# Kernel optimization log

Measured on AMD Instinct MI355X. Metric: run time of the kernel, lower is better.

## Reference

```python
import jax, jax.numpy as jnp
import numpy as np

B, T = 64, 64
HUMAN, IN = 64, 8
HS, ES, K = 1024, 1024, 7
PSI_H, PSI_LR = 1024, 30

_PAR_SHAPES = [(HS, HS), (HS,), (IN, HS), (HS, HUMAN), (IN, HUMAN - IN)]
_PAR_SIZES = [int(np.prod(s)) for s in _PAR_SHAPES]
N_PSI = int(sum(_PAR_SIZES))
_OFFS = np.cumsum([0] + _PAR_SIZES)


def setup_inputs() -> dict:
    key = jax.random.key(0)
    ks = jax.random.split(key, 16)
    def xav(k, shape):
        lim = float(np.sqrt(6.0 / (shape[0] + shape[1])))
        return jax.random.uniform(k, shape, minval=-lim, maxval=lim, dtype=jnp.float32)
    def uni(k, shape, s):
        return jax.random.uniform(k, shape, minval=-s, maxval=s, dtype=jnp.float32)
    se = float(1.0 / np.sqrt(ES))
    return {
        "inputs": jax.random.normal(ks[0], (B, T, IN), jnp.float32),
        "outputs": jax.random.normal(ks[1], (B, T, HUMAN), jnp.float32),
        "eps": jax.random.normal(ks[2], (B, K), jnp.float32),
        "enc_Wih": uni(ks[3], (3 * ES, HUMAN), se),
        "enc_Whh": uni(ks[4], (3 * ES, ES), se),
        "enc_bih": uni(ks[5], (3 * ES,), se),
        "enc_bhh": uni(ks[6], (3 * ES,), se),
        "to_mu": xav(ks[7], (ES, K)),
        "to_lsigma": xav(ks[8], (ES, K)),
        "to_lsigma_bias": -0.5 * jnp.ones((K,), jnp.float32),
        "W1": xav(ks[9], (K, PSI_H)),
        "b1": jnp.zeros((PSI_H,), jnp.float32),
        "W2": xav(ks[10], (PSI_H, PSI_LR)),
        "b2": jnp.zeros((PSI_LR,), jnp.float32),
        "W3": xav(ks[11], (PSI_LR, N_PSI)),
        "b3": jnp.zeros((N_PSI,), jnp.float32),
        "gru_Wih": xav(ks[12], (IN, 2 * HS)),
        "gru_Whh": xav(ks[13], (HS, 2 * HS)),
        "gru_bias": jnp.concatenate([jnp.zeros((HS,)), jnp.ones((HS,))]).astype(jnp.float32),
    }


def _gru_cell(h, x, Wih, Whh, bih, bhh):
    # torch.nn.GRUCell math, gate order (r, z, n)
    gx = x @ Wih.T + bih
    gh = h @ Whh.T + bhh
    xr, xz, xn = jnp.split(gx, 3, axis=-1)
    hr, hz, hn = jnp.split(gh, 3, axis=-1)
    r = jax.nn.sigmoid(xr + hr)
    z = jax.nn.sigmoid(xz + hz)
    n = jnp.tanh(xn + r * hn)
    return (1.0 - z) * n + z * h


def _split_psi(psi):
    # psi: [B, N_PSI] -> per-sample (Whh, bh, Wih, C, D)
    return [psi[:, _OFFS[i]:_OFFS[i + 1]].reshape((-1,) + _PAR_SHAPES[i]) for i in range(5)]


def reference(inputs, outputs, eps, enc_Wih, enc_Whh, enc_bih, enc_bhh,
              to_mu, to_lsigma, to_lsigma_bias, W1, b1, W2, b2, W3, b3,
              gru_Wih, gru_Whh, gru_bias):
    bsz = inputs.shape[0]
    # ---- encoder: GRUCell over time-major outputs ----
    out_tm = jnp.swapaxes(outputs, 0, 1)  # [T, B, HUMAN]
    h0 = jnp.zeros((bsz, ES), inputs.dtype)
    h_enc = _gru_cell(h0, out_tm[0], enc_Wih, enc_Whh, enc_bih, enc_bhh)
    def enc_step(h, x):
        h = _gru_cell(h, x, enc_Wih, enc_Whh, enc_bih, enc_bhh)
        return h, None
    h_enc, _ = jax.lax.scan(enc_step, h_enc, out_tm[1:])
    mu = h_enc @ to_mu                       # [B, K]
    logstd = h_enc @ to_lsigma + to_lsigma_bias
    z = mu + eps * jnp.exp(logstd)
    # ---- hypernetwork psi decoder ----
    psi = (jnp.tanh(z @ W1 + b1) @ W2 + b2) @ W3 + b3   # [B, N_PSI]
    Whh_b, bh_b, Wih_b, C_b, D_b = _split_psi(psi)
    # ---- per-sample GRU decoder, vectorized over batch, scan over time ----
    gx_all = jnp.einsum('bti,ij->tbj', inputs, gru_Wih)  # [T, B, 2*HS]
    xW_all = jnp.einsum('bti,bih->tbh', inputs, Wih_b)   # [T, B, HS]

    def dec_step(h, xs):
        gx_t, xW_t = xs
        pre = gx_t + h @ gru_Whh + gru_bias   # [B, 2*HS]
        z_t = jax.nn.sigmoid(pre[:, :HS])
        r_t = jax.nn.sigmoid(pre[:, HS:])
        hWhh = jnp.einsum('bh,bhk->bk', h, Whh_b) + bh_b
        eta = jnp.tanh(xW_t + r_t * jnp.tanh(hWhh))
        h_new = z_t * h + (1.0 - z_t) * eta
        return h_new, h_new

    state0 = jnp.zeros((bsz, HS), inputs.dtype)
    h_last, dec_seq = jax.lax.scan(dec_step, state0, (gx_all, xW_all))
    dec_seq = jnp.swapaxes(dec_seq, 0, 1)    # [B, T, HS]
    # ---- readout ----
    yhats = jnp.einsum('bth,bhm->btm', dec_seq, C_b)
    xD = jnp.einsum('bti,bim->btm', inputs, D_b)  # [B, T, HUMAN-IN]
    yhats = yhats + jnp.concatenate([jnp.zeros_like(inputs), xD], axis=-1)
    # residual output
    yhats = yhats + jnp.concatenate(
        [inputs, jnp.zeros((bsz, inputs.shape[1], HUMAN - IN), inputs.dtype)], axis=-1)
    states = jax.lax.stop_gradient(h_last)
    return yhats, mu, logstd, states
```

## Files before the change

kernel.cpp:

```cpp
#include <hip/hip_runtime.h>

namespace {
constexpr int nT = 64;
constexpr int nK = 7;
constexpr long N_PSI = 1123776;
constexpr long SZ_WHH = 1048576;
constexpr long REST_SZ = 75200;
constexpr long R_BH = 0;
constexpr long R_WIH = 1024;
constexpr long R_C = 9216;
constexpr long R_D = 74752;
constexpr int NCH = 32;
constexpr int CHR = 32;
constexpr long PHALF = (long)NCH * 64 * 1024;
}

typedef __attribute__((ext_vector_type(4))) unsigned short us4;
typedef __attribute__((ext_vector_type(2))) unsigned short us2;

__device__ __forceinline__ float b2f(unsigned short u) {
  return __uint_as_float(((unsigned int)u) << 16);
}
__device__ __forceinline__ unsigned short f2b(float f) {
  unsigned int u = __float_as_uint(f);
  return (unsigned short)((u + 0x7fffu + ((u >> 16) & 1u)) >> 16);
}
__device__ __forceinline__ float sigm(float x) { return 1.f / (1.f + __expf(-x)); }

__global__ void transpose_bf16_k(const float* __restrict__ in, unsigned short* __restrict__ out,
                                 int rows, int cols) {
  __shared__ float tile[32][33];
  int x = blockIdx.x * 32 + threadIdx.x;
  int y = blockIdx.y * 32 + threadIdx.y;
  #pragma unroll
  for (int i = 0; i < 32; i += 8)
    if ((y + i) < rows && x < cols) tile[threadIdx.y + i][threadIdx.x] = in[(long)(y + i) * cols + x];
  __syncthreads();
  x = blockIdx.y * 32 + threadIdx.x;
  y = blockIdx.x * 32 + threadIdx.y;
  #pragma unroll
  for (int i = 0; i < 32; i += 8)
    if ((y + i) < cols && x < rows) out[(long)(y + i) * rows + x] = f2b(tile[threadIdx.x][threadIdx.y + i]);
}

__global__ void cvt_bf16_k(const float* __restrict__ in, unsigned short* __restrict__ out, long n) {
  long i = (long)blockIdx.x * 256 + threadIdx.x;
  if (i < n) out[i] = f2b(in[i]);
}

__global__ __launch_bounds__(256) void enc_gx_k(const float* __restrict__ outputs,
                                                const unsigned short* __restrict__ WtWihB,
                                                const float* __restrict__ bih,
                                                unsigned short* __restrict__ gxE) {
  int g0 = blockIdx.x * 256;
  int btg = blockIdx.y;
  __shared__ unsigned short ws[64 * 256];
  __shared__ float xs[64][64];
  for (int i = threadIdx.x; i < 64 * 256; i += 256)
    ws[i] = WtWihB[(long)(i >> 8) * 3072 + g0 + (i & 255)];
  for (int i = threadIdx.x; i < 64 * 64; i += 256) {
    int idx = btg * 64 + (i >> 6);
    int t = idx >> 6, b = idx & 63;
    xs[i >> 6][i & 63] = outputs[((long)b * nT + t) * 64 + (i & 63)];
  }
  __syncthreads();
  float bihv = bih[g0 + threadIdx.x];
  for (int j = 0; j < 64; ++j) {
    int idx = btg * 64 + j;
    float acc = bihv;
    #pragma unroll 8
    for (int i = 0; i < 64; ++i) acc += xs[j][i] * b2f(ws[i * 256 + threadIdx.x]);
    gxE[(long)idx * 3072 + g0 + threadIdx.x] = f2b(acc);
  }
}

__global__ __launch_bounds__(256) void dec_gx_k(const float* __restrict__ inputs,
                                                const float* __restrict__ gWih,
                                                const float* __restrict__ gbias,
                                                unsigned short* __restrict__ gxD) {
  int g0 = blockIdx.x * 256;
  int btg = blockIdx.y;
  __shared__ float ws[8][256];
  __shared__ float xs[64][8];
  for (int i = threadIdx.x; i < 8 * 256; i += 256)
    ws[i >> 8][i & 255] = gWih[(long)(i >> 8) * 2048 + g0 + (i & 255)];
  for (int i = threadIdx.x; i < 64 * 8; i += 256) {
    int idx = btg * 64 + (i >> 3);
    int t = idx >> 6, b = idx & 63;
    xs[i >> 3][i & 7] = inputs[((long)b * nT + t) * 8 + (i & 7)];
  }
  __syncthreads();
  float bv = gbias[g0 + threadIdx.x];
  for (int j = 0; j < 64; ++j) {
    int idx = btg * 64 + j;
    float acc = bv;
    #pragma unroll
    for (int i = 0; i < 8; ++i) acc += xs[j][i] * ws[i][threadIdx.x];
    gxD[(long)idx * 2048 + g0 + threadIdx.x] = f2b(acc);
  }
}

__global__ __launch_bounds__(256) void xW_k(const float* __restrict__ inputs,
                                            const float* __restrict__ Rest,
                                            unsigned short* __restrict__ xWb) {
  int k0 = blockIdx.x * 256;
  int b = blockIdx.y;
  __shared__ float ws[8][256];
  __shared__ float xs[64][8];
  const float* RB = Rest + (long)b * REST_SZ + R_WIH;
  for (int i = threadIdx.x; i < 8 * 256; i += 256)
    ws[i >> 8][i & 255] = RB[(long)(i >> 8) * 1024 + k0 + (i & 255)];
  for (int i = threadIdx.x; i < 64 * 8; i += 256)
    xs[i >> 3][i & 7] = inputs[((long)b * nT + (i >> 3)) * 8 + (i & 7)];
  __syncthreads();
  for (int t = 0; t < 64; ++t) {
    float acc = 0.f;
    #pragma unroll
    for (int i = 0; i < 8; ++i) acc += xs[t][i] * ws[i][threadIdx.x];
    xWb[((long)t * 64 + b) * 1024 + k0 + threadIdx.x] = f2b(acc);
  }
}

__global__ __launch_bounds__(256) void enc_step_k(
    const unsigned short* __restrict__ W,
    const unsigned short* __restrict__ gxE,
    const float* __restrict__ bhh,
    float* __restrict__ hEnc,
    const float* __restrict__ pRr, const float* __restrict__ pZr, const float* __restrict__ pNr,
    float* __restrict__ pRw, float* __restrict__ pZw, float* __restrict__ pNw,
    int t) {
  int c = blockIdx.x & (NCH - 1);
  int sp = blockIdx.x >> 5;
  int b0 = sp * 2, b1 = b0 + 1;
  __shared__ float h0s[CHR], h1s[CHR];
  __shared__ float redR[4][64], redZ[4][64], redN[4][64];

  int v = threadIdx.x;
  int q = v >> 6, idx = v & 63;
  {
    int hi = idx >> 5, e_in = idx & 31;
    int bb = hi ? b1 : b0;
    int e = c * CHR + e_in;
    float sr = 0.f, sz = 0.f, sn = 0.f;
    if (t > 0) {
      #pragma unroll
      for (int cc = q * 8; cc < q * 8 + 8; ++cc) {
        long base = ((long)cc * 64 + bb) * 1024 + e;
        sr += pRr[base]; sz += pZr[base]; sn += pNr[base];
      }
    }
    redR[q][idx] = sr; redZ[q][idx] = sz; redN[q][idx] = sn;
  }
  __syncthreads();
  if (v < 64) {
    int hi = v >> 5, e_in = v & 31;
    int bb = hi ? b1 : b0;
    int e = c * CHR + e_in;
    float sr = redR[0][v] + redR[1][v] + redR[2][v] + redR[3][v];
    float sz = redZ[0][v] + redZ[1][v] + redZ[2][v] + redZ[3][v];
    float sn = redN[0][v] + redN[1][v] + redN[2][v] + redN[3][v];
    long gb = ((long)t * 64 + bb) * 3072;
    float xr = b2f(gxE[gb + e]), xz = b2f(gxE[gb + 1024 + e]), xn = b2f(gxE[gb + 2048 + e]);
    float hr = sr + bhh[e], hz = sz + bhh[1024 + e], hn = sn + bhh[2048 + e];
    float r = sigm(xr + hr);
    float z = sigm(xz + hz);
    float n = tanhf(xn + r * hn);
    float hold = (t > 0) ? hEnc[(long)bb * 1024 + e] : 0.f;
    float hnew = (1.f - z) * n + z * hold;
    hEnc[(long)bb * 1024 + e] = hnew;
    if (hi) h1s[e_in] = hnew; else h0s[e_in] = hnew;
  }
  __syncthreads();

  if (t < nT - 1) {
    int e0 = threadIdx.x * 4;
    float ar0[4] = {}, az0[4] = {}, an0[4] = {}, ar1[4] = {}, az1[4] = {}, an1[4] = {};
    const unsigned short* Wb = W + (long)(c * CHR) * 3072 + e0;
    #pragma unroll 4
    for (int j = 0; j < CHR; ++j) {
      us4 wr = *(const us4*)(Wb + (long)j * 3072);
      us4 wz = *(const us4*)(Wb + (long)j * 3072 + 1024);
      us4 wn = *(const us4*)(Wb + (long)j * 3072 + 2048);
      float hv0 = h0s[j], hv1 = h1s[j];
      #pragma unroll
      for (int qq = 0; qq < 4; ++qq) {
        float fr = b2f(wr[qq]), fz = b2f(wz[qq]), fn = b2f(wn[qq]);
        ar0[qq] += hv0 * fr; az0[qq] += hv0 * fz; an0[qq] += hv0 * fn;
        ar1[qq] += hv1 * fr; az1[qq] += hv1 * fz; an1[qq] += hv1 * fn;
      }
    }
    long i0 = ((long)c * 64 + b0) * 1024 + e0;
    long i1 = i0 + 1024;
    *(float4*)(pRw + i0) = make_float4(ar0[0], ar0[1], ar0[2], ar0[3]);
    *(float4*)(pZw + i0) = make_float4(az0[0], az0[1], az0[2], az0[3]);
    *(float4*)(pNw + i0) = make_float4(an0[0], an0[1], an0[2], an0[3]);
    *(float4*)(pRw + i1) = make_float4(ar1[0], ar1[1], ar1[2], ar1[3]);
    *(float4*)(pZw + i1) = make_float4(az1[0], az1[1], az1[2], az1[3]);
    *(float4*)(pNw + i1) = make_float4(an1[0], an1[1], an1[2], an1[3]);
  }
}

__global__ __launch_bounds__(256) void latent_hyper_k(
    const float* __restrict__ h_enc,
    const float* __restrict__ to_mu, const float* __restrict__ to_lsig,
    const float* __restrict__ lsig_bias, const float* __restrict__ eps,
    const float* __restrict__ W1, const float* __restrict__ b1,
    const float* __restrict__ W2, const float* __restrict__ b2,
    float* __restrict__ out_mu, float* __restrict__ out_lsig,
    float* __restrict__ a2out) {
  int b = blockIdx.x;
  __shared__ float hs[1024];
  __shared__ float zv[8];
  __shared__ float a1[1024];
  for (int i = threadIdx.x; i < 1024; i += 256) hs[i] = h_enc[b * 1024 + i];
  __syncthreads();
  int g = threadIdx.x >> 5, s = threadIdx.x & 31;
  if (g < nK) {
    float am = 0.f, as_ = 0.f;
    for (int h = s; h < 1024; h += 32) {
      float hv = hs[h];
      am += hv * to_mu[h * nK + g];
      as_ += hv * to_lsig[h * nK + g];
    }
    #pragma unroll
    for (int m = 16; m >= 1; m >>= 1) { am += __shfl_xor(am, m); as_ += __shfl_xor(as_, m); }
    if (s == 0) {
      float ls = as_ + lsig_bias[g];
      out_mu[b * nK + g] = am;
      out_lsig[b * nK + g] = ls;
      zv[g] = am + eps[b * nK + g] * __expf(ls);
    }
  }
  __syncthreads();
  for (int j = threadIdx.x; j < 1024; j += 256) {
    float acc = b1[j];
    #pragma unroll
    for (int i = 0; i < nK; ++i) acc += zv[i] * W1[i * 1024 + j];
    a1[j] = tanhf(acc);
  }
  __syncthreads();
  int l = threadIdx.x >> 3, s8 = threadIdx.x & 7;
  if (l < 30) {
    float acc = 0.f;
    for (int j = s8; j < 1024; j += 8) acc += a1[j] * W2[j * 30 + l];
    acc += __shfl_xor(acc, 4);
    acc += __shfl_xor(acc, 2);
    acc += __shfl_xor(acc, 1);
    if (s8 == 0) a2out[b * 30 + l] = acc + b2[l];
  }
}

__global__ __launch_bounds__(256) void psi_k(const float* __restrict__ a2,
                                             const float* __restrict__ W3, const float* __restrict__ b3,
                                             unsigned short* __restrict__ WhhB, float* __restrict__ Rest) {
  __shared__ float sa[64 * 30];
  for (int i = threadIdx.x; i < 64 * 30; i += 256) sa[i] = a2[i];
  long n0 = ((long)blockIdx.x * 256 + threadIdx.x) * 2;
  __syncthreads();
  if (n0 >= N_PSI) return;
  float2 w[30];
  #pragma unroll
  for (int l = 0; l < 30; ++l) w[l] = *(const float2*)(W3 + (long)l * N_PSI + n0);
  float2 bb = *(const float2*)(b3 + n0);
  bool isWhh = (n0 < SZ_WHH);
  for (int b = 0; b < 64; ++b) {
    float a0 = bb.x, a1v = bb.y;
    const float* ab = &sa[b * 30];
    #pragma unroll
    for (int l = 0; l < 30; ++l) { float av = ab[l]; a0 += av * w[l].x; a1v += av * w[l].y; }
    if (isWhh) {
      us2 o; o[0] = f2b(a0); o[1] = f2b(a1v);
      *(us2*)(WhhB + (long)b * SZ_WHH + n0) = o;
    } else {
      *(float2*)(Rest + (long)b * REST_SZ + (n0 - SZ_WHH)) = make_float2(a0, a1v);
    }
  }
}

__global__ __launch_bounds__(256) void dec_step_k(
    const unsigned short* __restrict__ WhhB,
    const unsigned short* __restrict__ gWhhB,
    const unsigned short* __restrict__ gxD,
    const unsigned short* __restrict__ xWb,
    const float* __restrict__ Rest,
    float* __restrict__ decS,
    const float* __restrict__ pZr, const float* __restrict__ pRr, const float* __restrict__ pWr,
    float* __restrict__ pZw, float* __restrict__ pRw, float* __restrict__ pWw,
    int t) {
  int c = blockIdx.x & (NCH - 1);
  int sp = blockIdx.x >> 5;
  int b0 = sp * 2, b1 = b0 + 1;
  __shared__ float h0s[CHR], h1s[CHR];
  __shared__ float redZ[4][64], redR[4][64], redW[4][64];

  int v = threadIdx.x;
  int q = v >> 6, idx = v & 63;
  {
    int hi = idx >> 5, e_in = idx & 31;
    int bb = hi ? b1 : b0;
    int k = c * CHR + e_in;
    float sz = 0.f, sr = 0.f, sw = 0.f;
    if (t > 0) {
      #pragma unroll
      for (int cc = q * 8; cc < q * 8 + 8; ++cc) {
        long base = ((long)cc * 64 + bb) * 1024 + k;
        sz += pZr[base]; sr += pRr[base]; sw += pWr[base];
      }
    }
    redZ[q][idx] = sz; redR[q][idx] = sr; redW[q][idx] = sw;
  }
  __syncthreads();
  if (v < 64) {
    int hi = v >> 5, e_in = v & 31;
    int bb = hi ? b1 : b0;
    int k = c * CHR + e_in;
    float sz = redZ[0][v] + redZ[1][v] + redZ[2][v] + redZ[3][v];
    float sr = redR[0][v] + redR[1][v] + redR[2][v] + redR[3][v];
    float sw = redW[0][v] + redW[1][v] + redW[2][v] + redW[3][v];
    long gb = ((long)t * 64 + bb) * 2048;
    float gz = b2f(gxD[gb + k]), gr = b2f(gxD[gb + 1024 + k]);
    float z = sigm(gz + sz);
    float r = sigm(gr + sr);
    float hW = sw + Rest[(long)bb * REST_SZ + R_BH + k];
    float xw = b2f(xWb[((long)t * 64 + bb) * 1024 + k]);
    float eta = tanhf(xw + r * tanhf(hW));
    float hold = (t > 0) ? decS[((long)bb * nT + (t - 1)) * 1024 + k] : 0.f;
    float hnew = z * hold + (1.f - z) * eta;
    decS[((long)bb * nT + t) * 1024 + k] = hnew;
    if (hi) h1s[e_in] = hnew; else h0s[e_in] = hnew;
  }
  __syncthreads();

  if (t < nT - 1) {
    int k0 = threadIdx.x * 4;
    float az0[4] = {}, ar0[4] = {}, aw0[4] = {}, az1[4] = {}, ar1[4] = {}, aw1[4] = {};
    const unsigned short* G = gWhhB + (long)(c * CHR) * 2048 + k0;
    const unsigned short* W0 = WhhB + (long)b0 * SZ_WHH + (long)(c * CHR) * 1024 + k0;
    const unsigned short* W1p = WhhB + (long)b1 * SZ_WHH + (long)(c * CHR) * 1024 + k0;
    #pragma unroll 4
    for (int j = 0; j < CHR; ++j) {
      us4 wz = *(const us4*)(G + (long)j * 2048);
      us4 wr = *(const us4*)(G + (long)j * 2048 + 1024);
      us4 w0 = *(const us4*)(W0 + (long)j * 1024);
      us4 w1 = *(const us4*)(W1p + (long)j * 1024);
      float hv0 = h0s[j], hv1 = h1s[j];
      #pragma unroll
      for (int qq = 0; qq < 4; ++qq) {
        float fz = b2f(wz[qq]), fr = b2f(wr[qq]), f0 = b2f(w0[qq]), f1 = b2f(w1[qq]);
        az0[qq] += hv0 * fz; ar0[qq] += hv0 * fr; aw0[qq] += hv0 * f0;
        az1[qq] += hv1 * fz; ar1[qq] += hv1 * fr; aw1[qq] += hv1 * f1;
      }
    }
    long i0 = ((long)c * 64 + b0) * 1024 + k0;
    long i1 = i0 + 1024;
    *(float4*)(pZw + i0) = make_float4(az0[0], az0[1], az0[2], az0[3]);
    *(float4*)(pRw + i0) = make_float4(ar0[0], ar0[1], ar0[2], ar0[3]);
    *(float4*)(pWw + i0) = make_float4(aw0[0], aw0[1], aw0[2], aw0[3]);
    *(float4*)(pZw + i1) = make_float4(az1[0], az1[1], az1[2], az1[3]);
    *(float4*)(pRw + i1) = make_float4(ar1[0], ar1[1], ar1[2], ar1[3]);
    *(float4*)(pWw + i1) = make_float4(aw1[0], aw1[1], aw1[2], aw1[3]);
  }
}

__global__ __launch_bounds__(256) void readout_k(
    const float* __restrict__ dec_seq, const float* __restrict__ inputs,
    const float* __restrict__ Rest, float* __restrict__ yhats) {
  int b = blockIdx.x >> 3;
  int tg = blockIdx.x & 7;
  __shared__ float ss[8][1024];
  __shared__ float part[4][8][64];
  for (int i = threadIdx.x; i < 8 * 1024; i += 256)
    ss[i >> 10][i & 1023] = dec_seq[((long)b * nT + tg * 8 + (i >> 10)) * 1024 + (i & 1023)];
  __syncthreads();
  int m = threadIdx.x & 63, hq = threadIdx.x >> 6;
  const float* C = Rest + (long)b * REST_SZ + R_C;
  float acc[8] = {};
  for (int h = hq * 256; h < hq * 256 + 256; ++h) {
    float cv = C[(long)h * 64 + m];
    #pragma unroll
    for (int tt = 0; tt < 8; ++tt) acc[tt] += ss[tt][h] * cv;
  }
  #pragma unroll
  for (int tt = 0; tt < 8; ++tt) part[hq][tt][m] = acc[tt];
  __syncthreads();
  const float* D = Rest + (long)b * REST_SZ + R_D;
  for (int o = threadIdx.x; o < 512; o += 256) {
    int tt = o >> 6, mm = o & 63;
    float a = part[0][tt][mm] + part[1][tt][mm] + part[2][tt][mm] + part[3][tt][mm];
    long bt = (long)b * nT + tg * 8 + tt;
    if (mm < 8) {
      a += inputs[bt * 8 + mm];
    } else {
      #pragma unroll
      for (int i = 0; i < 8; ++i) a += inputs[bt * 8 + i] * D[i * 56 + (mm - 8)];
    }
    yhats[bt * 64 + mm] = a;
  }
}

__global__ void copy_states_k(const float* __restrict__ dec_seq, float* __restrict__ states) {
  int i = blockIdx.x * 256 + threadIdx.x;
  int b = i >> 10, h = i & 1023;
  states[i] = dec_seq[((long)b * nT + (nT - 1)) * 1024 + h];
}

extern "C" void kernel_launch(void* const* d_in, const int* in_sizes, int n_in,
                              void* d_out, int out_size, void* d_ws, size_t ws_size,
                              hipStream_t stream) {
  const float* inputs  = (const float*)d_in[0];
  const float* outputs = (const float*)d_in[1];
  const float* eps     = (const float*)d_in[2];
  const float* enc_Wih = (const float*)d_in[3];
  const float* enc_Whh = (const float*)d_in[4];
  const float* enc_bih = (const float*)d_in[5];
  const float* enc_bhh = (const float*)d_in[6];
  const float* to_mu   = (const float*)d_in[7];
  const float* to_lsig = (const float*)d_in[8];
  const float* lsig_b  = (const float*)d_in[9];
  const float* W1 = (const float*)d_in[10];
  const float* b1 = (const float*)d_in[11];
  const float* W2 = (const float*)d_in[12];
  const float* b2 = (const float*)d_in[13];
  const float* W3 = (const float*)d_in[14];
  const float* b3 = (const float*)d_in[15];
  const float* gWih  = (const float*)d_in[16];
  const float* gWhh  = (const float*)d_in[17];
  const float* gbias = (const float*)d_in[18];

  char* ws = (char*)d_ws;
  size_t off = 0;
  auto alloc = [&](size_t bytes) { size_t o = off; off = (off + bytes + 255) & ~(size_t)255; return o; };
  size_t oWhhB   = alloc(64ull * SZ_WHH * 2);
  size_t oRest   = alloc(64ull * REST_SZ * 4);
  size_t ogWhhB  = alloc(1024ull * 2048 * 2);
  size_t oWtWhhB = alloc(1024ull * 3072 * 2);
  size_t oWtWihB = alloc(64ull * 3072 * 2);
  size_t ogxE    = alloc(64ull * 64 * 3072 * 2);
  size_t ogxD    = alloc(64ull * 64 * 2048 * 2);
  size_t oxWb    = alloc(64ull * 64 * 1024 * 2);
  size_t opA     = alloc((size_t)2 * PHALF * 4);
  size_t opB     = alloc((size_t)2 * PHALF * 4);
  size_t opC     = alloc((size_t)2 * PHALF * 4);
  size_t ohA     = alloc(64ull * 1024 * 4);
  size_t oDec    = alloc(64ull * 64 * 1024 * 4);
  size_t oZ      = alloc(64 * nK * 4);
  size_t oA2     = alloc(64 * 30 * 4);
  (void)ws_size; (void)in_sizes; (void)n_in; (void)out_size; (void)oZ;

  unsigned short* WhhB   = (unsigned short*)(ws + oWhhB);
  float*          Rest   = (float*)(ws + oRest);
  unsigned short* gWhhB  = (unsigned short*)(ws + ogWhhB);
  unsigned short* WtWhhB = (unsigned short*)(ws + oWtWhhB);
  unsigned short* WtWihB = (unsigned short*)(ws + oWtWihB);
  unsigned short* gxE    = (unsigned short*)(ws + ogxE);
  unsigned short* gxD    = (unsigned short*)(ws + ogxD);
  unsigned short* xWb    = (unsigned short*)(ws + oxWb);
  float* pA   = (float*)(ws + opA);
  float* pB   = (float*)(ws + opB);
  float* pC   = (float*)(ws + opC);
  float* hA   = (float*)(ws + ohA);
  float* decS = (float*)(ws + oDec);
  float* a2   = (float*)(ws + oA2);

  float* out    = (float*)d_out;
  float* out_yh = out;
  float* out_mu = out + 262144;
  float* out_ls = out + 262144 + 448;
  float* out_st = out + 262144 + 896;

  transpose_bf16_k<<<dim3(32, 96), dim3(32, 8), 0, stream>>>(enc_Whh, WtWhhB, 3072, 1024);
  transpose_bf16_k<<<dim3(2, 96),  dim3(32, 8), 0, stream>>>(enc_Wih, WtWihB, 3072, 64);
  cvt_bf16_k<<<(int)((1024ull * 2048 + 255) / 256), 256, 0, stream>>>(gWhh, gWhhB, 1024 * 2048);

  enc_gx_k<<<dim3(12, 64), 256, 0, stream>>>(outputs, WtWihB, enc_bih, gxE);

  for (int t = 0; t < nT; ++t) {
    int rp = t & 1, wp = (t + 1) & 1;
    enc_step_k<<<1024, 256, 0, stream>>>(WtWhhB, gxE, enc_bhh, hA,
        pA + (size_t)rp * PHALF, pB + (size_t)rp * PHALF, pC + (size_t)rp * PHALF,
        pA + (size_t)wp * PHALF, pB + (size_t)wp * PHALF, pC + (size_t)wp * PHALF, t);
  }

  latent_hyper_k<<<64, 256, 0, stream>>>(hA, to_mu, to_lsig, lsig_b, eps,
                                         W1, b1, W2, b2, out_mu, out_ls, a2);
  psi_k<<<(int)((N_PSI / 2 + 255) / 256), 256, 0, stream>>>(a2, W3, b3, WhhB, Rest);

  dec_gx_k<<<dim3(8, 64), 256, 0, stream>>>(inputs, gWih, gbias, gxD);
  xW_k<<<dim3(4, 64), 256, 0, stream>>>(inputs, Rest, xWb);

  for (int t = 0; t < nT; ++t) {
    int rp = t & 1, wp = (t + 1) & 1;
    dec_step_k<<<1024, 256, 0, stream>>>(WhhB, gWhhB, gxD, xWb, Rest, decS,
        pA + (size_t)rp * PHALF, pB + (size_t)rp * PHALF, pC + (size_t)rp * PHALF,
        pA + (size_t)wp * PHALF, pB + (size_t)wp * PHALF, pC + (size_t)wp * PHALF, t);
  }

  readout_k<<<512, 256, 0, stream>>>(decS, inputs, Rest, out_yh);
  copy_states_k<<<256, 256, 0, stream>>>(decS, out_st);
}
```

Baseline: 3.401 ms.

## Restructure decoder step into per-sample and shared-weight block groups; widen encoder chunks

The encoder step now uses 16 chunks of 64 rows instead of 32 of 32. This halves the partial-sum buffers and the cross-chunk reduction reads, and drops the shared-memory reduction stage. The decoder step is rewritten. 256 blocks each handle one sample and a quarter of the per-sample hypernetwork Whh product, with all 1024 rows reduced inside the block. Another 128 blocks compute the shared GRU gate product for groups of 8 samples, so gWhh is reused across those samples. Each block recomputes the full hidden-state update redundantly to avoid the partial-sum reduction, and the per-block serial loops are longer with fewer blocks.

```diff
diff --git a/kernel.cpp b/kernel.cpp
--- a/kernel.cpp
+++ b/kernel.cpp
@@ -10,9 +10,9 @@
 constexpr long R_WIH = 1024;
 constexpr long R_C = 9216;
 constexpr long R_D = 74752;
-constexpr int NCH = 32;
-constexpr int CHR = 32;
-constexpr long PHALF = (long)NCH * 64 * 1024;
+constexpr int NCHE = 16;
+constexpr int CHRE = 64;
+constexpr long PHALF_E = (long)NCHE * 64 * 1024;
 }
 
 typedef __attribute__((ext_vector_type(4))) unsigned short us4;
@@ -129,36 +129,24 @@
     const float* __restrict__ pRr, const float* __restrict__ pZr, const float* __restrict__ pNr,
     float* __restrict__ pRw, float* __restrict__ pZw, float* __restrict__ pNw,
     int t) {
-  int c = blockIdx.x & (NCH - 1);
-  int sp = blockIdx.x >> 5;
+  int c = blockIdx.x & (NCHE - 1);
+  int sp = blockIdx.x >> 4;
   int b0 = sp * 2, b1 = b0 + 1;
-  __shared__ float h0s[CHR], h1s[CHR];
-  __shared__ float redR[4][64], redZ[4][64], redN[4][64];
+  __shared__ float h0s[CHRE], h1s[CHRE];
 
   int v = threadIdx.x;
-  int q = v >> 6, idx = v & 63;
-  {
-    int hi = idx >> 5, e_in = idx & 31;
+  if (v < 2 * CHRE) {
+    int hi = v >> 6;
     int bb = hi ? b1 : b0;
-    int e = c * CHR + e_in;
+    int e = c * CHRE + (v & 63);
     float sr = 0.f, sz = 0.f, sn = 0.f;
     if (t > 0) {
       #pragma unroll
-      for (int cc = q * 8; cc < q * 8 + 8; ++cc) {
+      for (int cc = 0; cc < NCHE; ++cc) {
         long base = ((long)cc * 64 + bb) * 1024 + e;
         sr += pRr[base]; sz += pZr[base]; sn += pNr[base];
       }
     }
-    redR[q][idx] = sr; redZ[q][idx] = sz; redN[q][idx] = sn;
-  }
-  __syncthreads();
-  if (v < 64) {
-    int hi = v >> 5, e_in = v & 31;
-    int bb = hi ? b1 : b0;
-    int e = c * CHR + e_in;
-    float sr = redR[0][v] + redR[1][v] + redR[2][v] + redR[3][v];
-    float sz = redZ[0][v] + redZ[1][v] + redZ[2][v] + redZ[3][v];
-    float sn = redN[0][v] + redN[1][v] + redN[2][v] + redN[3][v];
     long gb = ((long)t * 64 + bb) * 3072;
     float xr = b2f(gxE[gb + e]), xz = b2f(gxE[gb + 1024 + e]), xn = b2f(gxE[gb + 2048 + e]);
     float hr = sr + bhh[e], hz = sz + bhh[1024 + e], hn = sn + bhh[2048 + e];
@@ -168,25 +156,25 @@
     float hold = (t > 0) ? hEnc[(long)bb * 1024 + e] : 0.f;
     float hnew = (1.f - z) * n + z * hold;
     hEnc[(long)bb * 1024 + e] = hnew;
-    if (hi) h1s[e_in] = hnew; else h0s[e_in] = hnew;
+    if (hi) h1s[v & 63] = hnew; else h0s[v & 63] = hnew;
   }
   __syncthreads();
 
   if (t < nT - 1) {
     int e0 = threadIdx.x * 4;
     float ar0[4] = {}, az0[4] = {}, an0[4] = {}, ar1[4] = {}, az1[4] = {}, an1[4] = {};
-    const unsigned short* Wb = W + (long)(c * CHR) * 3072 + e0;
+    const unsigned short* Wb = W + (long)(c * CHRE) * 3072 + e0;
     #pragma unroll 4
-    for (int j = 0; j < CHR; ++j) {
+    for (int j = 0; j < CHRE; ++j) {
       us4 wr = *(const us4*)(Wb + (long)j * 3072);
       us4 wz = *(const us4*)(Wb + (long)j * 3072 + 1024);
       us4 wn = *(const us4*)(Wb + (long)j * 3072 + 2048);
       float hv0 = h0s[j], hv1 = h1s[j];
       #pragma unroll
-      for (int qq = 0; qq < 4; ++qq) {
-        float fr = b2f(wr[qq]), fz = b2f(wz[qq]), fn = b2f(wn[qq]);
-        ar0[qq] += hv0 * fr; az0[qq] += hv0 * fz; an0[qq] += hv0 * fn;
-        ar1[qq] += hv1 * fr; az1[qq] += hv1 * fz; an1[qq] += hv1 * fn;
+      for (int q = 0; q < 4; ++q) {
+        float fr = b2f(wr[q]), fz = b2f(wz[q]), fn = b2f(wn[q]);
+        ar0[q] += hv0 * fr; az0[q] += hv0 * fz; an0[q] += hv0 * fn;
+        ar1[q] += hv1 * fr; az1[q] += hv1 * fz; an1[q] += hv1 * fn;
       }
     }
     long i0 = ((long)c * 64 + b0) * 1024 + e0;
@@ -277,88 +265,101 @@
   }
 }
 
-__global__ __launch_bounds__(256) void dec_step_k(
+__global__ __launch_bounds__(256) void dec_step2_k(
     const unsigned short* __restrict__ WhhB,
     const unsigned short* __restrict__ gWhhB,
     const unsigned short* __restrict__ gxD,
     const unsigned short* __restrict__ xWb,
     const float* __restrict__ Rest,
     float* __restrict__ decS,
-    const float* __restrict__ pZr, const float* __restrict__ pRr, const float* __restrict__ pWr,
-    float* __restrict__ pZw, float* __restrict__ pRw, float* __restrict__ pWw,
+    const float* __restrict__ hWr, const float* __restrict__ preR,
+    float* __restrict__ hWw, float* __restrict__ preW,
     int t) {
-  int c = blockIdx.x & (NCH - 1);
-  int sp = blockIdx.x >> 5;
-  int b0 = sp * 2, b1 = b0 + 1;
-  __shared__ float h0s[CHR], h1s[CHR];
-  __shared__ float redZ[4][64], redR[4][64], redW[4][64];
-
-  int v = threadIdx.x;
-  int q = v >> 6, idx = v & 63;
-  {
-    int hi = idx >> 5, e_in = idx & 31;
-    int bb = hi ? b1 : b0;
-    int k = c * CHR + e_in;
-    float sz = 0.f, sr = 0.f, sw = 0.f;
-    if (t > 0) {
+  int blk = blockIdx.x;
+  int tid = threadIdx.x;
+  if (blk < 256) {
+    int b = blk >> 2, kq = blk & 3;
+    __shared__ float hs[1024];
+    __shared__ float part[4][64][4];
+    {
+      int kk = tid * 4;
+      float4 hold = make_float4(0.f, 0.f, 0.f, 0.f);
+      if (t > 0) hold = *(const float4*)(decS + ((long)b * nT + (t - 1)) * 1024 + kk);
+      const float* bh = Rest + (long)b * REST_SZ + R_BH;
+      long gb = ((long)t * 64 + b) * 2048;
+      long xb = ((long)t * 64 + b) * 1024;
+      float hv[4]; float ho[4] = {hold.x, hold.y, hold.z, hold.w};
       #pragma unroll
-      for (int cc = q * 8; cc < q * 8 + 8; ++cc) {
-        long base = ((long)cc * 64 + bb) * 1024 + k;
-        sz += pZr[base]; sr += pRr[base]; sw += pWr[base];
+      for (int q = 0; q < 4; ++q) {
+        int k = kk + q;
+        float pz = 0.f, pr = 0.f, hw = 0.f;
+        if (t > 0) {
+          pz = preR[(long)b * 2048 + k];
+          pr = preR[(long)b * 2048 + 1024 + k];
+          hw = hWr[(long)b * 1024 + k];
+        }
+        float z = sigm(b2f(gxD[gb + k]) + pz);
+        float r = sigm(b2f(gxD[gb + 1024 + k]) + pr);
+        float eta = tanhf(b2f(xWb[xb + k]) + r * tanhf(hw + bh[k]));
+        hv[q] = z * ho[q] + (1.f - z) * eta;
       }
-    }
-    redZ[q][idx] = sz; redR[q][idx] = sr; redW[q][idx] = sw;
-  }
-  __syncthreads();
-  if (v < 64) {
-    int hi = v >> 5, e_in = v & 31;
-    int bb = hi ? b1 : b0;
-    int k = c * CHR + e_in;
-    float sz = redZ[0][v] + redZ[1][v] + redZ[2][v] + redZ[3][v];
-    float sr = redR[0][v] + redR[1][v] + redR[2][v] + redR[3][v];
-    float sw = redW[0][v] + redW[1][v] + redW[2][v] + redW[3][v];
-    long gb = ((long)t * 64 + bb) * 2048;
-    float gz = b2f(gxD[gb + k]), gr = b2f(gxD[gb + 1024 + k]);
-    float z = sigm(gz + sz);
-    float r = sigm(gr + sr);
-    float hW = sw + Rest[(long)bb * REST_SZ + R_BH + k];
-    float xw = b2f(xWb[((long)t * 64 + bb) * 1024 + k]);
-    float eta = tanhf(xw + r * tanhf(hW));
-    float hold = (t > 0) ? decS[((long)bb * nT + (t - 1)) * 1024 + k] : 0.f;
-    float hnew = z * hold + (1.f - z) * eta;
-    decS[((long)bb * nT + t) * 1024 + k] = hnew;
-    if (hi) h1s[e_in] = hnew; else h0s[e_in] = hnew;
-  }
-  __syncthreads();
-
-  if (t < nT - 1) {
-    int k0 = threadIdx.x * 4;
-    float az0[4] = {}, ar0[4] = {}, aw0[4] = {}, az1[4] = {}, ar1[4] = {}, aw1[4] = {};
-    const unsigned short* G = gWhhB + (long)(c * CHR) * 2048 + k0;
-    const unsigned short* W0 = WhhB + (long)b0 * SZ_WHH + (long)(c * CHR) * 1024 + k0;
-    const unsigned short* W1p = WhhB + (long)b1 * SZ_WHH + (long)(c * CHR) * 1024 + k0;
-    #pragma unroll 4
-    for (int j = 0; j < CHR; ++j) {
-      us4 wz = *(const us4*)(G + (long)j * 2048);
-      us4 wr = *(const us4*)(G + (long)j * 2048 + 1024);
-      us4 w0 = *(const us4*)(W0 + (long)j * 1024);
-      us4 w1 = *(const us4*)(W1p + (long)j * 1024);
-      float hv0 = h0s[j], hv1 = h1s[j];
-      #pragma unroll
-      for (int qq = 0; qq < 4; ++qq) {
-        float fz = b2f(wz[qq]), fr = b2f(wr[qq]), f0 = b2f(w0[qq]), f1 = b2f(w1[qq]);
-        az0[qq] += hv0 * fz; ar0[qq] += hv0 * fr; aw0[qq] += hv0 * f0;
-        az1[qq] += hv1 * fz; ar1[qq] += hv1 * fr; aw1[qq] += hv1 * f1;
+      *(float4*)(hs + kk) = make_float4(hv[0], hv[1], hv[2], hv[3]);
+      if ((tid >> 6) == kq)
+        *(float4*)(decS + ((long)b * nT + t) * 1024 + kk) = make_float4(hv[0], hv[1], hv[2], hv[3]);
+    }
+    __syncthreads();
+    if (t < nT - 1) {
+      int lane = tid & 63, hq = tid >> 6;
+      int k0 = kq * 256 + lane * 4;
+      const unsigned short* W = WhhB + (long)b * SZ_WHH + k0;
+      float a0 = 0.f, a1 = 0.f, a2v = 0.f, a3 = 0.f;
+      for (int h = hq; h < 1024; h += 4) {
+        us4 w = *(const us4*)(W + (long)h * 1024);
+        float hv = hs[h];
+        a0 += hv * b2f(w[0]); a1 += hv * b2f(w[1]); a2v += hv * b2f(w[2]); a3 += hv * b2f(w[3]);
       }
-    }
-    long i0 = ((long)c * 64 + b0) * 1024 + k0;
-    long i1 = i0 + 1024;
-    *(float4*)(pZw + i0) = make_float4(az0[0], az0[1], az0[2], az0[3]);
-    *(float4*)(pRw + i0) = make_float4(ar0[0], ar0[1], ar0[2], ar0[3]);
-    *(float4*)(pWw + i0) = make_float4(aw0[0], aw0[1], aw0[2], aw0[3]);
-    *(float4*)(pZw + i1) = make_float4(az1[0], az1[1], az1[2], az1[3]);
-    *(float4*)(pRw + i1) = make_float4(ar1[0], ar1[1], ar1[2], ar1[3]);
-    *(float4*)(pWw + i1) = make_float4(aw1[0], aw1[1], aw1[2], aw1[3]);
+      part[hq][lane][0] = a0; part[hq][lane][1] = a1; part[hq][lane][2] = a2v; part[hq][lane][3] = a3;
+      __syncthreads();
+      float s = part[0][tid >> 2][tid & 3] + part[1][tid >> 2][tid & 3]
+              + part[2][tid >> 2][tid & 3] + part[3][tid >> 2][tid & 3];
+      hWw[(long)b * 1024 + kq * 256 + tid] = s;
+    }
+  } else {
+    int g = blk - 256;
+    int sg = g >> 4, gq = g & 15;
+    int s0 = sg * 8;
+    __shared__ float hs8[8][1024];
+    for (int i = tid; i < 8192; i += 256) {
+      int s = i >> 10, k = i & 1023;
+      int b = s0 + s;
+      float hold = (t > 0) ? decS[((long)b * nT + (t - 1)) * 1024 + k] : 0.f;
+      float pz = 0.f, pr = 0.f, hw = 0.f;
+      if (t > 0) {
+        pz = preR[(long)b * 2048 + k];
+        pr = preR[(long)b * 2048 + 1024 + k];
+        hw = hWr[(long)b * 1024 + k];
+      }
+      long gb = ((long)t * 64 + b) * 2048;
+      float z = sigm(b2f(gxD[gb + k]) + pz);
+      float r = sigm(b2f(gxD[gb + 1024 + k]) + pr);
+      float eta = tanhf(b2f(xWb[((long)t * 64 + b) * 1024 + k])
+                        + r * tanhf(hw + Rest[(long)b * REST_SZ + R_BH + k]));
+      hs8[s][k] = z * hold + (1.f - z) * eta;
+    }
+    __syncthreads();
+    if (t < nT - 1) {
+      int s = tid >> 5;
+      int b = s0 + s;
+      int cc = gq * 128 + (tid & 31) * 4;
+      const unsigned short* G = gWhhB + cc;
+      float a0 = 0.f, a1 = 0.f, a2v = 0.f, a3 = 0.f;
+      for (int h = 0; h < 1024; ++h) {
+        us4 w = *(const us4*)(G + (long)h * 2048);
+        float hv = hs8[s][h];
+        a0 += hv * b2f(w[0]); a1 += hv * b2f(w[1]); a2v += hv * b2f(w[2]); a3 += hv * b2f(w[3]);
+      }
+      *(float4*)(preW + (long)b * 2048 + cc) = make_float4(a0, a1, a2v, a3);
+    }
   }
 }
 
@@ -438,14 +439,15 @@
   size_t ogxE    = alloc(64ull * 64 * 3072 * 2);
   size_t ogxD    = alloc(64ull * 64 * 2048 * 2);
   size_t oxWb    = alloc(64ull * 64 * 1024 * 2);
-  size_t opA     = alloc((size_t)2 * PHALF * 4);
-  size_t opB     = alloc((size_t)2 * PHALF * 4);
-  size_t opC     = alloc((size_t)2 * PHALF * 4);
+  size_t opA     = alloc((size_t)2 * PHALF_E * 4);
+  size_t opB     = alloc((size_t)2 * PHALF_E * 4);
+  size_t opC     = alloc((size_t)2 * PHALF_E * 4);
   size_t ohA     = alloc(64ull * 1024 * 4);
+  size_t oHW     = alloc((size_t)2 * 64 * 1024 * 4);
+  size_t oPre    = alloc((size_t)2 * 64 * 2048 * 4);
   size_t oDec    = alloc(64ull * 64 * 1024 * 4);
-  size_t oZ      = alloc(64 * nK * 4);
   size_t oA2     = alloc(64 * 30 * 4);
-  (void)ws_size; (void)in_sizes; (void)n_in; (void)out_size; (void)oZ;
+  (void)ws_size; (void)in_sizes; (void)n_in; (void)out_size;
 
   unsigned short* WhhB   = (unsigned short*)(ws + oWhhB);
   float*          Rest   = (float*)(ws + oRest);
@@ -459,6 +461,8 @@
   float* pB   = (float*)(ws + opB);
   float* pC   = (float*)(ws + opC);
   float* hA   = (float*)(ws + ohA);
+  float* hW   = (float*)(ws + oHW);
+  float* pre  = (float*)(ws + oPre);
   float* decS = (float*)(ws + oDec);
   float* a2   = (float*)(ws + oA2);
 
@@ -476,9 +480,9 @@
 
   for (int t = 0; t < nT; ++t) {
     int rp = t & 1, wp = (t + 1) & 1;
-    enc_step_k<<<1024, 256, 0, stream>>>(WtWhhB, gxE, enc_bhh, hA,
-        pA + (size_t)rp * PHALF, pB + (size_t)rp * PHALF, pC + (size_t)rp * PHALF,
-        pA + (size_t)wp * PHALF, pB + (size_t)wp * PHALF, pC + (size_t)wp * PHALF, t);
+    enc_step_k<<<512, 256, 0, stream>>>(WtWhhB, gxE, enc_bhh, hA,
+        pA + (size_t)rp * PHALF_E, pB + (size_t)rp * PHALF_E, pC + (size_t)rp * PHALF_E,
+        pA + (size_t)wp * PHALF_E, pB + (size_t)wp * PHALF_E, pC + (size_t)wp * PHALF_E, t);
   }
 
   latent_hyper_k<<<64, 256, 0, stream>>>(hA, to_mu, to_lsig, lsig_b, eps,
@@ -490,9 +494,9 @@
 
   for (int t = 0; t < nT; ++t) {
     int rp = t & 1, wp = (t + 1) & 1;
-    dec_step_k<<<1024, 256, 0, stream>>>(WhhB, gWhhB, gxD, xWb, Rest, decS,
-        pA + (size_t)rp * PHALF, pB + (size_t)rp * PHALF, pC + (size_t)rp * PHALF,
-        pA + (size_t)wp * PHALF, pB + (size_t)wp * PHALF, pC + (size_t)wp * PHALF, t);
+    dec_step2_k<<<384, 256, 0, stream>>>(WhhB, gWhhB, gxD, xWb, Rest, decS,
+        hW + (size_t)rp * 65536, pre + (size_t)rp * 131072,
+        hW + (size_t)wp * 65536, pre + (size_t)wp * 131072, t);
   }
 
   readout_k<<<512, 256, 0, stream>>>(decS, inputs, Rest, out_yh);
```

After: 7.722 ms. +127.0%, slower.

## Quantize per-sample decoder Whh to int8 and halve the recurrent chunk count

Applied to the files above, without the earlier changes.

Adds a pass after the hypernetwork that computes per-column absmax scales and quantizes each sample's generated 1024x1024 Whh from bf16 to int8. The decoder step then streams int8 weights and applies the scale after accumulation, roughly halving the dominant per-step weight traffic. Separately, both encoder and decoder step kernels use 16 chunks of 64 rows instead of 32 of 32. This halves the grid, drops the shared-memory partial reduction, and lets each reducing thread sum all chunks directly. The int8 quantization adds numerical error to the recurrence and depends on workspace size, falling back to bf16 otherwise.

```diff
diff --git a/kernel.cpp b/kernel.cpp
--- a/kernel.cpp
+++ b/kernel.cpp
@@ -10,8 +10,8 @@
 constexpr long R_WIH = 1024;
 constexpr long R_C = 9216;
 constexpr long R_D = 74752;
-constexpr int NCH = 32;
-constexpr int CHR = 32;
+constexpr int NCH = 16;
+constexpr int CHR = 64;
 constexpr long PHALF = (long)NCH * 64 * 1024;
 }
 
@@ -130,35 +130,23 @@
     float* __restrict__ pRw, float* __restrict__ pZw, float* __restrict__ pNw,
     int t) {
   int c = blockIdx.x & (NCH - 1);
-  int sp = blockIdx.x >> 5;
+  int sp = blockIdx.x >> 4;
   int b0 = sp * 2, b1 = b0 + 1;
   __shared__ float h0s[CHR], h1s[CHR];
-  __shared__ float redR[4][64], redZ[4][64], redN[4][64];
 
   int v = threadIdx.x;
-  int q = v >> 6, idx = v & 63;
-  {
-    int hi = idx >> 5, e_in = idx & 31;
+  if (v < 2 * CHR) {
+    int hi = v >> 6;
     int bb = hi ? b1 : b0;
-    int e = c * CHR + e_in;
+    int e = c * CHR + (v & 63);
     float sr = 0.f, sz = 0.f, sn = 0.f;
     if (t > 0) {
       #pragma unroll
-      for (int cc = q * 8; cc < q * 8 + 8; ++cc) {
+      for (int cc = 0; cc < NCH; ++cc) {
         long base = ((long)cc * 64 + bb) * 1024 + e;
         sr += pRr[base]; sz += pZr[base]; sn += pNr[base];
       }
     }
-    redR[q][idx] = sr; redZ[q][idx] = sz; redN[q][idx] = sn;
-  }
-  __syncthreads();
-  if (v < 64) {
-    int hi = v >> 5, e_in = v & 31;
-    int bb = hi ? b1 : b0;
-    int e = c * CHR + e_in;
-    float sr = redR[0][v] + redR[1][v] + redR[2][v] + redR[3][v];
-    float sz = redZ[0][v] + redZ[1][v] + redZ[2][v] + redZ[3][v];
-    float sn = redN[0][v] + redN[1][v] + redN[2][v] + redN[3][v];
     long gb = ((long)t * 64 + bb) * 3072;
     float xr = b2f(gxE[gb + e]), xz = b2f(gxE[gb + 1024 + e]), xn = b2f(gxE[gb + 2048 + e]);
     float hr = sr + bhh[e], hz = sz + bhh[1024 + e], hn = sn + bhh[2048 + e];
@@ -168,7 +156,7 @@
     float hold = (t > 0) ? hEnc[(long)bb * 1024 + e] : 0.f;
     float hnew = (1.f - z) * n + z * hold;
     hEnc[(long)bb * 1024 + e] = hnew;
-    if (hi) h1s[e_in] = hnew; else h0s[e_in] = hnew;
+    if (hi) h1s[v & 63] = hnew; else h0s[v & 63] = hnew;
   }
   __syncthreads();
 
@@ -183,10 +171,10 @@
       us4 wn = *(const us4*)(Wb + (long)j * 3072 + 2048);
       float hv0 = h0s[j], hv1 = h1s[j];
       #pragma unroll
-      for (int qq = 0; qq < 4; ++qq) {
-        float fr = b2f(wr[qq]), fz = b2f(wz[qq]), fn = b2f(wn[qq]);
-        ar0[qq] += hv0 * fr; az0[qq] += hv0 * fz; an0[qq] += hv0 * fn;
-        ar1[qq] += hv1 * fr; az1[qq] += hv1 * fz; an1[qq] += hv1 * fn;
+      for (int q = 0; q < 4; ++q) {
+        float fr = b2f(wr[q]), fz = b2f(wz[q]), fn = b2f(wn[q]);
+        ar0[q] += hv0 * fr; az0[q] += hv0 * fz; an0[q] += hv0 * fn;
+        ar1[q] += hv1 * fr; az1[q] += hv1 * fz; an1[q] += hv1 * fn;
       }
     }
     long i0 = ((long)c * 64 + b0) * 1024 + e0;
@@ -277,7 +265,148 @@
   }
 }
 
-__global__ __launch_bounds__(256) void dec_step_k(
+__global__ __launch_bounds__(256) void wmax_k(const unsigned short* __restrict__ WhhB,
+                                              float* __restrict__ pmax) {
+  int b = blockIdx.x >> 2, rq = blockIdx.x & 3;
+  int k0 = threadIdx.x * 4;
+  float m0 = 0.f, m1 = 0.f, m2 = 0.f, m3 = 0.f;
+  const unsigned short* W = WhhB + (long)b * SZ_WHH + (long)rq * 256 * 1024 + k0;
+  #pragma unroll 4
+  for (int j = 0; j < 256; ++j) {
+    us4 w = *(const us4*)(W + (long)j * 1024);
+    m0 = fmaxf(m0, fabsf(b2f(w[0])));
+    m1 = fmaxf(m1, fabsf(b2f(w[1])));
+    m2 = fmaxf(m2, fabsf(b2f(w[2])));
+    m3 = fmaxf(m3, fabsf(b2f(w[3])));
+  }
+  *(float4*)(pmax + ((long)b * 4 + rq) * 1024 + k0) = make_float4(m0, m1, m2, m3);
+}
+
+__global__ __launch_bounds__(256) void wscale_k(const float* __restrict__ pmax,
+                                                float* __restrict__ wsc) {
+  int b = blockIdx.x;
+  int k0 = threadIdx.x * 4;
+  float4 a = *(const float4*)(pmax + ((long)b * 4 + 0) * 1024 + k0);
+  float4 c = *(const float4*)(pmax + ((long)b * 4 + 1) * 1024 + k0);
+  float4 d = *(const float4*)(pmax + ((long)b * 4 + 2) * 1024 + k0);
+  float4 e = *(const float4*)(pmax + ((long)b * 4 + 3) * 1024 + k0);
+  float m0 = fmaxf(fmaxf(a.x, c.x), fmaxf(d.x, e.x));
+  float m1 = fmaxf(fmaxf(a.y, c.y), fmaxf(d.y, e.y));
+  float m2 = fmaxf(fmaxf(a.z, c.z), fmaxf(d.z, e.z));
+  float m3 = fmaxf(fmaxf(a.w, c.w), fmaxf(d.w, e.w));
+  float s0 = (m0 > 0.f) ? m0 / 127.f : 1.f;
+  float s1 = (m1 > 0.f) ? m1 / 127.f : 1.f;
+  float s2 = (m2 > 0.f) ? m2 / 127.f : 1.f;
+  float s3 = (m3 > 0.f) ? m3 / 127.f : 1.f;
+  *(float4*)(wsc + (long)b * 1024 + k0) = make_float4(s0, s1, s2, s3);
+}
+
+__global__ __launch_bounds__(256) void wquant_k(const unsigned short* __restrict__ WhhB,
+                                                const float* __restrict__ wsc,
+                                                char* __restrict__ Q8) {
+  int b = blockIdx.x >> 2, rq = blockIdx.x & 3;
+  int k0 = threadIdx.x * 4;
+  float4 s = *(const float4*)(wsc + (long)b * 1024 + k0);
+  float i0 = 1.f / s.x, i1 = 1.f / s.y, i2 = 1.f / s.z, i3 = 1.f / s.w;
+  const unsigned short* W = WhhB + (long)b * SZ_WHH + (long)rq * 256 * 1024 + k0;
+  char* Q = Q8 + (long)b * SZ_WHH + (long)rq * 256 * 1024 + k0;
+  #pragma unroll 4
+  for (int j = 0; j < 256; ++j) {
+    us4 w = *(const us4*)(W + (long)j * 1024);
+    int q0 = __float2int_rn(b2f(w[0]) * i0);
+    int q1 = __float2int_rn(b2f(w[1]) * i1);
+    int q2 = __float2int_rn(b2f(w[2]) * i2);
+    int q3 = __float2int_rn(b2f(w[3]) * i3);
+    q0 = min(127, max(-127, q0)); q1 = min(127, max(-127, q1));
+    q2 = min(127, max(-127, q2)); q3 = min(127, max(-127, q3));
+    *(char4*)(Q + (long)j * 1024) = make_char4((char)q0, (char)q1, (char)q2, (char)q3);
+  }
+}
+
+__global__ __launch_bounds__(256) void dec_step_q8_k(
+    const char* __restrict__ Q8,
+    const float* __restrict__ Wsc,
+    const unsigned short* __restrict__ gWhhB,
+    const unsigned short* __restrict__ gxD,
+    const unsigned short* __restrict__ xWb,
+    const float* __restrict__ Rest,
+    float* __restrict__ decS,
+    const float* __restrict__ pZr, const float* __restrict__ pRr, const float* __restrict__ pWr,
+    float* __restrict__ pZw, float* __restrict__ pRw, float* __restrict__ pWw,
+    int t) {
+  int c = blockIdx.x & (NCH - 1);
+  int sp = blockIdx.x >> 4;
+  int b0 = sp * 2, b1 = b0 + 1;
+  __shared__ float h0s[CHR], h1s[CHR];
+
+  int v = threadIdx.x;
+  if (v < 2 * CHR) {
+    int hi = v >> 6;
+    int bb = hi ? b1 : b0;
+    int k = c * CHR + (v & 63);
+    float sz = 0.f, sr = 0.f, sw = 0.f;
+    float hold = 0.f;
+    if (t > 0) {
+      #pragma unroll
+      for (int cc = 0; cc < NCH; ++cc) {
+        long base = ((long)cc * 64 + bb) * 1024 + k;
+        sz += pZr[base]; sr += pRr[base]; sw += pWr[base];
+      }
+      hold = decS[((long)bb * nT + (t - 1)) * 1024 + k];
+    }
+    long gb = ((long)t * 64 + bb) * 2048;
+    float gz = b2f(gxD[gb + k]), gr = b2f(gxD[gb + 1024 + k]);
+    float z = sigm(gz + sz);
+    float r = sigm(gr + sr);
+    float hW = sw + Rest[(long)bb * REST_SZ + R_BH + k];
+    float xw = b2f(xWb[((long)t * 64 + bb) * 1024 + k]);
+    float eta = tanhf(xw + r * tanhf(hW));
+    float hnew = z * hold + (1.f - z) * eta;
+    decS[((long)bb * nT + t) * 1024 + k] = hnew;
+    if (hi) h1s[v & 63] = hnew; else h0s[v & 63] = hnew;
+  }
+  __syncthreads();
+
+  if (t < nT - 1) {
+    int k0 = threadIdx.x * 4;
+    float az0[4] = {}, ar0[4] = {}, aw0[4] = {}, az1[4] = {}, ar1[4] = {}, aw1[4] = {};
+    const unsigned short* G = gWhhB + (long)(c * CHR) * 2048 + k0;
+    const char* Q0 = Q8 + (long)b0 * SZ_WHH + (long)(c * CHR) * 1024 + k0;
+    const char* Q1 = Q8 + (long)b1 * SZ_WHH + (long)(c * CHR) * 1024 + k0;
+    #pragma unroll 4
+    for (int j = 0; j < CHR; ++j) {
+      us4 wz = *(const us4*)(G + (long)j * 2048);
+      us4 wr = *(const us4*)(G + (long)j * 2048 + 1024);
+      char4 q0 = *(const char4*)(Q0 + (long)j * 1024);
+      char4 q1 = *(const char4*)(Q1 + (long)j * 1024);
+      float hv0 = h0s[j], hv1 = h1s[j];
+      float f00 = (float)q0.x, f01 = (float)q0.y, f02 = (float)q0.z, f03 = (float)q0.w;
+      float f10 = (float)q1.x, f11 = (float)q1.y, f12 = (float)q1.z, f13 = (float)q1.w;
+      #pragma unroll
+      for (int q = 0; q < 4; ++q) {
+        float fz = b2f(wz[q]), fr = b2f(wr[q]);
+        az0[q] += hv0 * fz; ar0[q] += hv0 * fr;
+        az1[q] += hv1 * fz; ar1[q] += hv1 * fr;
+      }
+      aw0[0] += hv0 * f00; aw0[1] += hv0 * f01; aw0[2] += hv0 * f02; aw0[3] += hv0 * f03;
+      aw1[0] += hv1 * f10; aw1[1] += hv1 * f11; aw1[2] += hv1 * f12; aw1[3] += hv1 * f13;
+    }
+    float4 s0v = *(const float4*)(Wsc + (long)b0 * 1024 + k0);
+    float4 s1v = *(const float4*)(Wsc + (long)b1 * 1024 + k0);
+    aw0[0] *= s0v.x; aw0[1] *= s0v.y; aw0[2] *= s0v.z; aw0[3] *= s0v.w;
+    aw1[0] *= s1v.x; aw1[1] *= s1v.y; aw1[2] *= s1v.z; aw1[3] *= s1v.w;
+    long i0 = ((long)c * 64 + b0) * 1024 + k0;
+    long i1 = i0 + 1024;
+    *(float4*)(pZw + i0) = make_float4(az0[0], az0[1], az0[2], az0[3]);
+    *(float4*)(pRw + i0) = make_float4(ar0[0], ar0[1], ar0[2], ar0[3]);
+    *(float4*)(pWw + i0) = make_float4(aw0[0], aw0[1], aw0[2], aw0[3]);
+    *(float4*)(pZw + i1) = make_float4(az1[0], az1[1], az1[2], az1[3]);
+    *(float4*)(pRw + i1) = make_float4(ar1[0], ar1[1], ar1[2], ar1[3]);
+    *(float4*)(pWw + i1) = make_float4(aw1[0], aw1[1], aw1[2], aw1[3]);
+  }
+}
+
+__global__ __launch_bounds__(256) void dec_step_bf_k(
     const unsigned short* __restrict__ WhhB,
     const unsigned short* __restrict__ gWhhB,
     const unsigned short* __restrict__ gxD,
@@ -288,35 +417,25 @@
     float* __restrict__ pZw, float* __restrict__ pRw, float* __restrict__ pWw,
     int t) {
   int c = blockIdx.x & (NCH - 1);
-  int sp = blockIdx.x >> 5;
+  int sp = blockIdx.x >> 4;
   int b0 = sp * 2, b1 = b0 + 1;
   __shared__ float h0s[CHR], h1s[CHR];
-  __shared__ float redZ[4][64], redR[4][64], redW[4][64];
 
   int v = threadIdx.x;
-  int q = v >> 6, idx = v & 63;
-  {
-    int hi = idx >> 5, e_in = idx & 31;
+  if (v < 2 * CHR) {
+    int hi = v >> 6;
     int bb = hi ? b1 : b0;
-    int k = c * CHR + e_in;
+    int k = c * CHR + (v & 63);
     float sz = 0.f, sr = 0.f, sw = 0.f;
+    float hold = 0.f;
     if (t > 0) {
       #pragma unroll
-      for (int cc = q * 8; cc < q * 8 + 8; ++cc) {
+      for (int cc = 0; cc < NCH; ++cc) {
         long base = ((long)cc * 64 + bb) * 1024 + k;
         sz += pZr[base]; sr += pRr[base]; sw += pWr[base];
       }
-    }
-    redZ[q][idx] = sz; redR[q][idx] = sr; redW[q][idx] = sw;
-  }
-  __syncthreads();
-  if (v < 64) {
-    int hi = v >> 5, e_in = v & 31;
-    int bb = hi ? b1 : b0;
-    int k = c * CHR + e_in;
-    float sz = redZ[0][v] + redZ[1][v] + redZ[2][v] + redZ[3][v];
-    float sr = redR[0][v] + redR[1][v] + redR[2][v] + redR[3][v];
-    float sw = redW[0][v] + redW[1][v] + redW[2][v] + redW[3][v];
+      hold = decS[((long)bb * nT + (t - 1)) * 1024 + k];
+    }
     long gb = ((long)t * 64 + bb) * 2048;
     float gz = b2f(gxD[gb + k]), gr = b2f(gxD[gb + 1024 + k]);
     float z = sigm(gz + sz);
@@ -324,10 +443,9 @@
     float hW = sw + Rest[(long)bb * REST_SZ + R_BH + k];
     float xw = b2f(xWb[((long)t * 64 + bb) * 1024 + k]);
     float eta = tanhf(xw + r * tanhf(hW));
-    float hold = (t > 0) ? decS[((long)bb * nT + (t - 1)) * 1024 + k] : 0.f;
     float hnew = z * hold + (1.f - z) * eta;
     decS[((long)bb * nT + t) * 1024 + k] = hnew;
-    if (hi) h1s[e_in] = hnew; else h0s[e_in] = hnew;
+    if (hi) h1s[v & 63] = hnew; else h0s[v & 63] = hnew;
   }
   __syncthreads();
 
@@ -345,10 +463,10 @@
       us4 w1 = *(const us4*)(W1p + (long)j * 1024);
       float hv0 = h0s[j], hv1 = h1s[j];
       #pragma unroll
-      for (int qq = 0; qq < 4; ++qq) {
-        float fz = b2f(wz[qq]), fr = b2f(wr[qq]), f0 = b2f(w0[qq]), f1 = b2f(w1[qq]);
-        az0[qq] += hv0 * fz; ar0[qq] += hv0 * fr; aw0[qq] += hv0 * f0;
-        az1[qq] += hv1 * fz; ar1[qq] += hv1 * fr; aw1[qq] += hv1 * f1;
+      for (int q = 0; q < 4; ++q) {
+        float fz = b2f(wz[q]), fr = b2f(wr[q]), f0 = b2f(w0[q]), f1 = b2f(w1[q]);
+        az0[q] += hv0 * fz; ar0[q] += hv0 * fr; aw0[q] += hv0 * f0;
+        az1[q] += hv1 * fz; ar1[q] += hv1 * fr; aw1[q] += hv1 * f1;
       }
     }
     long i0 = ((long)c * 64 + b0) * 1024 + k0;
@@ -443,9 +561,12 @@
   size_t opC     = alloc((size_t)2 * PHALF * 4);
   size_t ohA     = alloc(64ull * 1024 * 4);
   size_t oDec    = alloc(64ull * 64 * 1024 * 4);
-  size_t oZ      = alloc(64 * nK * 4);
   size_t oA2     = alloc(64 * 30 * 4);
-  (void)ws_size; (void)in_sizes; (void)n_in; (void)out_size; (void)oZ;
+  size_t oQ8     = alloc(64ull * SZ_WHH);
+  size_t oPmax   = alloc(64ull * 4 * 1024 * 4);
+  size_t oWsc    = alloc(64ull * 1024 * 4);
+  bool useQ8 = (off <= ws_size);
+  (void)in_sizes; (void)n_in; (void)out_size;
 
   unsigned short* WhhB   = (unsigned short*)(ws + oWhhB);
   float*          Rest   = (float*)(ws + oRest);
@@ -461,6 +582,9 @@
   float* hA   = (float*)(ws + ohA);
   float* decS = (float*)(ws + oDec);
   float* a2   = (float*)(ws + oA2);
+  char*  Q8   = (char*)(ws + oQ8);
+  float* pmax = (float*)(ws + oPmax);
+  float* wsc  = (float*)(ws + oWsc);
 
   float* out    = (float*)d_out;
   float* out_yh = out;
@@ -476,7 +600,7 @@
 
   for (int t = 0; t < nT; ++t) {
     int rp = t & 1, wp = (t + 1) & 1;
-    enc_step_k<<<1024, 256, 0, stream>>>(WtWhhB, gxE, enc_bhh, hA,
+    enc_step_k<<<512, 256, 0, stream>>>(WtWhhB, gxE, enc_bhh, hA,
         pA + (size_t)rp * PHALF, pB + (size_t)rp * PHALF, pC + (size_t)rp * PHALF,
         pA + (size_t)wp * PHALF, pB + (size_t)wp * PHALF, pC + (size_t)wp * PHALF, t);
   }
@@ -485,14 +609,26 @@
                                          W1, b1, W2, b2, out_mu, out_ls, a2);
   psi_k<<<(int)((N_PSI / 2 + 255) / 256), 256, 0, stream>>>(a2, W3, b3, WhhB, Rest);
 
+  if (useQ8) {
+    wmax_k<<<256, 256, 0, stream>>>(WhhB, pmax);
+    wscale_k<<<64, 256, 0, stream>>>(pmax, wsc);
+    wquant_k<<<256, 256, 0, stream>>>(WhhB, wsc, Q8);
+  }
+
   dec_gx_k<<<dim3(8, 64), 256, 0, stream>>>(inputs, gWih, gbias, gxD);
   xW_k<<<dim3(4, 64), 256, 0, stream>>>(inputs, Rest, xWb);
 
   for (int t = 0; t < nT; ++t) {
     int rp = t & 1, wp = (t + 1) & 1;
-    dec_step_k<<<1024, 256, 0, stream>>>(WhhB, gWhhB, gxD, xWb, Rest, decS,
-        pA + (size_t)rp * PHALF, pB + (size_t)rp * PHALF, pC + (size_t)rp * PHALF,
-        pA + (size_t)wp * PHALF, pB + (size_t)wp * PHALF, pC + (size_t)wp * PHALF, t);
+    if (useQ8) {
+      dec_step_q8_k<<<512, 256, 0, stream>>>(Q8, wsc, gWhhB, gxD, xWb, Rest, decS,
+          pA + (size_t)rp * PHALF, pB + (size_t)rp * PHALF, pC + (size_t)rp * PHALF,
+          pA + (size_t)wp * PHALF, pB + (size_t)wp * PHALF, pC + (size_t)wp * PHALF, t);
+    } else {
+      dec_step_bf_k<<<512, 256, 0, stream>>>(WhhB, gWhhB, gxD, xWb, Rest, decS,
+          pA + (size_t)rp * PHALF, pB + (size_t)rp * PHALF, pC + (size_t)rp * PHALF,
+          pA + (size_t)wp * PHALF, pB + (size_t)wp * PHALF, pC + (size_t)wp * PHALF, t);
+    }
   }
 
   readout_k<<<512, 256, 0, stream>>>(decS, inputs, Rest, out_yh);
```

After: 2.989 ms. -12.1%, faster.
